# Performance work log

Measured on AMD Instinct MI355X. Metric: run time of the kernel, lower is better.

## Reference

```python
import jax, jax.numpy as jnp
import numpy as np

T, B, E, H = 1024, 2, 1024, 16
D = E // H


def setup_inputs() -> dict:
    key = jax.random.key(0)
    ks = jax.random.split(key, 5)
    s = 1.0 / np.sqrt(E)  # xavier_uniform bound ~ sqrt(6/(fan_in+fan_out)); scale suffices for a numeric baseline
    return {
        "query": jax.random.normal(ks[0], (T, B, E), jnp.float32),
        "key_": jax.random.normal(ks[1], (T, B, E), jnp.float32),
        "value": jax.random.normal(ks[2], (T, B, E), jnp.float32),
        "in_proj_weight": jax.random.uniform(ks[3], (3 * E, E), jnp.float32, -s, s),
        "in_proj_bias": jnp.zeros((3 * E,), jnp.float32),
        "out_proj_weight": jax.random.uniform(ks[4], (E, E), jnp.float32, -s, s),
        "out_proj_bias": jnp.zeros((E,), jnp.float32),
    }


def reference(query, key_, value, in_proj_weight, in_proj_bias, out_proj_weight, out_proj_bias):
    # Faithful to CumulativeLinearMultiheadAttentionKV.forward with
    # batch_first=False, is_causal=True, no padding mask, no kv cache.
    Tl, Bl, El = query.shape
    wq, wk, wv = jnp.split(in_proj_weight, 3, axis=0)
    bq, bk, bv = jnp.split(in_proj_bias, 3)
    q = query @ wq.T + bq          # (T, B, E)
    k = key_ @ wk.T + bk
    v = value @ wv.T + bv

    def to_bhtd(x):
        return x.reshape(Tl, Bl, H, D).transpose(1, 2, 0, 3)  # (B, H, T, D)

    q, k, v = to_bhtd(q), to_bhtd(k), to_bhtd(v)

    scale = 1.0 / np.sqrt(D)  # SDPA-style default scale (scale=None)
    # cumulative linear attention: prefix sums of k_s \otimes v_s
    kv = jnp.einsum('bhsk,bhsv->bhskv', k, v)        # (B, H, T, D, D)
    kv_store = jnp.cumsum(kv, axis=2)                # causal KV state per step
    out = jnp.einsum('bhtk,bhtkv->bhtv', q, kv_store) * scale  # (B, H, T, D)

    out = out.transpose(2, 0, 1, 3).reshape(Tl, Bl, El)  # back to (T, B, E)
    out = out @ out_proj_weight.T + out_proj_bias
    return out
```

## Files before the change

### kernel.cpp

```cpp
#include <hip/hip_runtime.h>


#define E_DIM 1024

typedef short bf16x8 __attribute__((ext_vector_type(8)));
typedef float f32x4  __attribute__((ext_vector_type(4)));

__device__ inline unsigned short f2bf(float f) {
    unsigned u = __builtin_bit_cast(unsigned, f);
    u = (u + 0x7FFFu + ((u >> 16) & 1u)) >> 16;
    return (unsigned short)u;
}

__device__ inline void gload_lds16(const void* g, void* l) {
    __builtin_amdgcn_global_load_lds(
        (const __attribute__((address_space(1))) unsigned int*)g,
        (__attribute__((address_space(3))) unsigned int*)l, 16, 0, 0);
}

__device__ inline int swzb(int row, int colbyte) {
    return colbyte ^ ((row & 7) << 4);
}

__global__ __launch_bounds__(256) void k_castw(
    const float* __restrict__ w_in, const float* __restrict__ w_out,
    unsigned short* __restrict__ dst)
{
    const int id8 = blockIdx.x * 256 + threadIdx.x;
    const int WI8 = 3 * E_DIM * E_DIM / 8;
    const float* src = (id8 < WI8) ? (w_in + (size_t)id8 * 8)
                                   : (w_out + (size_t)(id8 - WI8) * 8);
    float4 f0 = *reinterpret_cast<const float4*>(src);
    float4 f1 = *reinterpret_cast<const float4*>(src + 4);
    ushort4 o0, o1;
    o0.x = f2bf(f0.x); o0.y = f2bf(f0.y); o0.z = f2bf(f0.z); o0.w = f2bf(f0.w);
    o1.x = f2bf(f1.x); o1.y = f2bf(f1.y); o1.z = f2bf(f1.z); o1.w = f2bf(f1.w);
    *reinterpret_cast<ushort4*>(dst + (size_t)id8 * 8)     = o0;
    *reinterpret_cast<ushort4*>(dst + (size_t)id8 * 8 + 4) = o1;
}

__global__ __launch_bounds__(256) void k_gin(
    const float* __restrict__ q_in, const float* __restrict__ k_in,
    const float* __restrict__ v_in, const unsigned short* __restrict__ Wibf,
    const float* __restrict__ b_in,
    unsigned short* __restrict__ qslab, unsigned short* __restrict__ kslab,
    unsigned short* __restrict__ ktb,   unsigned short* __restrict__ vtb)
{
    const int i = blockIdx.x;
    const int tile = (i & 7) * 48 + (i >> 3);
    const int z = tile >> 7;
    const int rem = tile & 127;
    const int x = rem >> 5, y = rem & 31;

    const float* X = (z == 0) ? q_in : (z == 1 ? k_in : v_in);
    const unsigned short* W = Wibf + (size_t)z * 1048576;
    const float* bz = b_in + z * E_DIM;

    const int nBase = x * 256;
    const int mBase = y * 64;
    const int b = mBase >> 10, tBase = mBase & 1023;

    __shared__ short As[2][64 * 64];
    __shared__ short Bs[2][256 * 64];

    const int tid = threadIdx.x;
    const int lane = tid & 63, wave = tid >> 6;
    const int wr = wave >> 1, wc = wave & 1;
    const int l15 = lane & 15, l4 = lane >> 4;

    auto stage = [&](int bufI, int k0) {
        #pragma unroll
        for (int l = 0; l < 8; ++l) {
            int off = l * 4096 + tid * 16;
            int row = off >> 7, cb = off & 127;
            gload_lds16((const char*)W + ((size_t)(nBase + row) * E_DIM + k0) * 2
                            + swzb(row, cb),
                        (char*)&Bs[bufI][0] + off);
        }
        #pragma unroll
        for (int l = 0; l < 2; ++l) {
            int u = tid + 256 * l;
            int row = u >> 3, cslot = u & 7;
            const float* src = &X[(size_t)((tBase + row) * 2 + b) * E_DIM
                                  + k0 + cslot * 8];
            float4 f0 = *reinterpret_cast<const float4*>(src);
            float4 f1 = *reinterpret_cast<const float4*>(src + 4);
            bf16x8 p;
            p[0] = (short)f2bf(f0.x); p[1] = (short)f2bf(f0.y);
            p[2] = (short)f2bf(f0.z); p[3] = (short)f2bf(f0.w);
            p[4] = (short)f2bf(f1.x); p[5] = (short)f2bf(f1.y);
            p[6] = (short)f2bf(f1.z); p[7] = (short)f2bf(f1.w);
            *reinterpret_cast<bf16x8*>(
                &As[bufI][row * 64 + (swzb(row, cslot * 16) >> 1)]) = p;
        }
    };

    f32x4 acc[2][8] = {};

    stage(0, 0);
    __syncthreads();
    int cur = 0;
    for (int it = 0; it < 16; ++it) {
        if (it < 15) stage(cur ^ 1, (it + 1) * 64);
        #pragma unroll
        for (int kk = 0; kk < 64; kk += 32) {
            bf16x8 af[2], bfr[8];
            #pragma unroll
            for (int ii = 0; ii < 2; ++ii) {
                int row = wr * 32 + ii * 16 + l15;
                af[ii] = *reinterpret_cast<const bf16x8*>(
                    &As[cur][row * 64 + (swzb(row, (kk + l4 * 8) * 2) >> 1)]);
            }
            #pragma unroll
            for (int j = 0; j < 8; ++j) {
                int row = wc * 128 + j * 16 + l15;
                bfr[j] = *reinterpret_cast<const bf16x8*>(
                    &Bs[cur][row * 64 + (swzb(row, (kk + l4 * 8) * 2) >> 1)]);
            }
            #pragma unroll
            for (int ii = 0; ii < 2; ++ii)
                #pragma unroll
                for (int j = 0; j < 8; ++j)
                    acc[ii][j] = __builtin_amdgcn_mfma_f32_16x16x32_bf16(
                        af[ii], bfr[j], acc[ii][j], 0, 0, 0);
        }
        __syncthreads();
        cur ^= 1;
    }

    #pragma unroll
    for (int ii = 0; ii < 2; ++ii) {
        int t0 = tBase + wr * 32 + ii * 16 + l4 * 4;
        #pragma unroll
        for (int j = 0; j < 8; ++j) {
            int col = nBase + wc * 128 + j * 16 + l15;
            float bv = bz[col];
            unsigned short v4[4];
            #pragma unroll
            for (int q = 0; q < 4; ++q) v4[q] = f2bf(acc[ii][j][q] + bv);
            if (z == 0) {
                #pragma unroll
                for (int q = 0; q < 4; ++q)
                    qslab[(size_t)b * 1048576 + (size_t)(t0 + q) * E_DIM + col] = v4[q];
            } else if (z == 1) {
                #pragma unroll
                for (int q = 0; q < 4; ++q)
                    kslab[(size_t)b * 1048576 + (size_t)(t0 + q) * E_DIM + col] = v4[q];
                ushort4 w = {v4[0], v4[1], v4[2], v4[3]};
                *reinterpret_cast<ushort4*>(
                    &ktb[((size_t)b * 1024 + col) * 1024 + t0]) = w;
            } else {
                ushort4 w = {v4[0], v4[1], v4[2], v4[3]};
                *reinterpret_cast<ushort4*>(
                    &vtb[((size_t)b * 1024 + col) * 1024 + t0]) = w;
            }
        }
    }
}

__global__ __launch_bounds__(256) void k_attn(
    const unsigned short* __restrict__ qslab, const unsigned short* __restrict__ kslab,
    const unsigned short* __restrict__ ktb,  const unsigned short* __restrict__ vtb,
    unsigned short* __restrict__ attnbf)
{
    const int i = blockIdx.x;
    const int xcd = i & 7, u = i >> 3;
    const int bh = xcd * 4 + (u >> 4);
    const int qtr = u & 15;
    const int qt = ((u >> 5) & 1) ? (15 - qtr) : qtr;
    const int b = bh >> 4, h = bh & 15;
    const int colb = h * 64, t0q = qt * 64;

    __shared__ short Qs[64 * 64];
    __shared__ short KB[2][64 * 64];
    __shared__ short VB[2][64 * 64];
    __shared__ short Ss[64 * 72];
    __shared__ short PTs[64 * 72];

    const int tid = threadIdx.x;
    const int lane = tid & 63, wave = tid >> 6;
    const int wr = wave >> 1, wc = wave & 1;
    const int l15 = lane & 15, l4 = lane >> 4;

    auto stageP = [&](int bufI, int c) {
        int t0k = c * 64;
        #pragma unroll
        for (int l = 0; l < 2; ++l) {
            int off = l * 4096 + tid * 16;
            int row = off >> 7, cb = off & 127;
            int scb = swzb(row, cb);
            size_t trn = ((size_t)(b * 1024 + colb + row)) * 1024 + t0k;
            gload_lds16((const char*)ktb + trn * 2 + scb, (char*)&KB[bufI][0] + off);
            gload_lds16((const char*)vtb + trn * 2 + scb, (char*)&VB[bufI][0] + off);
        }
    };
    auto stageDiag = [&](int bufI) {
        #pragma unroll
        for (int l = 0; l < 2; ++l) {
            int off = l * 4096 + tid * 16;
            int row = off >> 7, cb = off & 127;
            int scb = swzb(row, cb);
            gload_lds16((const char*)kslab +
                            ((size_t)b * 1048576 + (size_t)(t0q + row) * E_DIM + colb) * 2 + scb,
                        (char*)&KB[bufI][0] + off);
            gload_lds16((const char*)vtb +
                            (((size_t)(b * 1024 + colb + row)) * 1024 + t0q) * 2 + scb,
                        (char*)&VB[bufI][0] + off);
        }
    };

    #pragma unroll
    for (int l = 0; l < 2; ++l) {
        int off = l * 4096 + tid * 16;
        int row = off >> 7, cb = off & 127;
        gload_lds16((const char*)qslab +
                        ((size_t)b * 1048576 + (size_t)(t0q + row) * E_DIM + colb) * 2
                        + swzb(row, cb),
                    (char*)Qs + off);
    }
    if (qt > 0) stageP(0, 0); else stageDiag(0);
    __syncthreads();

    f32x4 pacc[2][2] = {};
    int cur = 0;

    for (int c = 0; c < qt; ++c) {
        if (c + 1 < qt) stageP(cur ^ 1, c + 1); else stageDiag(cur ^ 1);
        #pragma unroll
        for (int kk = 0; kk < 64; kk += 32) {
            bf16x8 af[2], bfr[2];
            #pragma unroll
            for (int ii = 0; ii < 2; ++ii) {
                int row = wr * 32 + ii * 16 + l15;
                af[ii] = *reinterpret_cast<const bf16x8*>(
                    &KB[cur][row * 64 + (swzb(row, (kk + l4 * 8) * 2) >> 1)]);
            }
            #pragma unroll
            for (int j = 0; j < 2; ++j) {
                int row = wc * 32 + j * 16 + l15;
                bfr[j] = *reinterpret_cast<const bf16x8*>(
                    &VB[cur][row * 64 + (swzb(row, (kk + l4 * 8) * 2) >> 1)]);
            }
            #pragma unroll
            for (int ii = 0; ii < 2; ++ii)
                #pragma unroll
                for (int j = 0; j < 2; ++j)
                    pacc[ii][j] = __builtin_amdgcn_mfma_f32_16x16x32_bf16(
                        af[ii], bfr[j], pacc[ii][j], 0, 0, 0);
        }
        __syncthreads();
        cur ^= 1;
    }

    f32x4 sacc[2][2] = {};
    #pragma unroll
    for (int kk = 0; kk < 64; kk += 32) {
        bf16x8 af[2], bfr[2];
        #pragma unroll
        for (int ii = 0; ii < 2; ++ii) {
            int row = wr * 32 + ii * 16 + l15;
            af[ii] = *reinterpret_cast<const bf16x8*>(
                &Qs[row * 64 + (swzb(row, (kk + l4 * 8) * 2) >> 1)]);
        }
        #pragma unroll
        for (int j = 0; j < 2; ++j) {
            int row = wc * 32 + j * 16 + l15;
            bfr[j] = *reinterpret_cast<const bf16x8*>(
                &KB[cur][row * 64 + (swzb(row, (kk + l4 * 8) * 2) >> 1)]);
        }
        #pragma unroll
        for (int ii = 0; ii < 2; ++ii)
            #pragma unroll
            for (int j = 0; j < 2; ++j)
                sacc[ii][j] = __builtin_amdgcn_mfma_f32_16x16x32_bf16(
                    af[ii], bfr[j], sacc[ii][j], 0, 0, 0);
    }

    #pragma unroll
    for (int ii = 0; ii < 2; ++ii) {
        #pragma unroll
        for (int j = 0; j < 2; ++j) {
            int dv = wc * 32 + j * 16 + l15;
            int dkb = wr * 32 + ii * 16 + l4 * 4;
            ushort4 pw;
            pw.x = f2bf(pacc[ii][j][0]); pw.y = f2bf(pacc[ii][j][1]);
            pw.z = f2bf(pacc[ii][j][2]); pw.w = f2bf(pacc[ii][j][3]);
            *reinterpret_cast<ushort4*>(&PTs[dv * 72 + dkb]) = pw;
            int kr = dv;
            #pragma unroll
            for (int q = 0; q < 4; ++q) {
                int qr = dkb + q;
                Ss[qr * 72 + kr] = (kr <= qr) ? (short)f2bf(sacc[ii][j][q]) : (short)0;
            }
        }
    }
    __syncthreads();

    f32x4 oacc[2][2] = {};
    #pragma unroll
    for (int kk = 0; kk < 64; kk += 32) {
        bf16x8 af[2], bfr[2];
        #pragma unroll
        for (int ii = 0; ii < 2; ++ii)
            af[ii] = *reinterpret_cast<const bf16x8*>(
                        &Ss[(wr * 32 + ii * 16 + l15) * 72 + kk + l4 * 8]);
        #pragma unroll
        for (int j = 0; j < 2; ++j) {
            int row = wc * 32 + j * 16 + l15;
            bfr[j] = *reinterpret_cast<const bf16x8*>(
                &VB[cur][row * 64 + (swzb(row, (kk + l4 * 8) * 2) >> 1)]);
        }
        #pragma unroll
        for (int ii = 0; ii < 2; ++ii)
            #pragma unroll
            for (int j = 0; j < 2; ++j)
                oacc[ii][j] = __builtin_amdgcn_mfma_f32_16x16x32_bf16(
                    af[ii], bfr[j], oacc[ii][j], 0, 0, 0);
    }
    #pragma unroll
    for (int kk = 0; kk < 64; kk += 32) {
        bf16x8 af[2], bfr[2];
        #pragma unroll
        for (int ii = 0; ii < 2; ++ii) {
            int row = wr * 32 + ii * 16 + l15;
            af[ii] = *reinterpret_cast<const bf16x8*>(
                &Qs[row * 64 + (swzb(row, (kk + l4 * 8) * 2) >> 1)]);
        }
        #pragma unroll
        for (int j = 0; j < 2; ++j)
            bfr[j] = *reinterpret_cast<const bf16x8*>(
                        &PTs[(wc * 32 + j * 16 + l15) * 72 + kk + l4 * 8]);
        #pragma unroll
        for (int ii = 0; ii < 2; ++ii)
            #pragma unroll
            for (int j = 0; j < 2; ++j)
                oacc[ii][j] = __builtin_amdgcn_mfma_f32_16x16x32_bf16(
                    af[ii], bfr[j], oacc[ii][j], 0, 0, 0);
    }

    #pragma unroll
    for (int ii = 0; ii < 2; ++ii) {
        #pragma unroll
        for (int j = 0; j < 2; ++j) {
            int dv = wc * 32 + j * 16 + l15;
            #pragma unroll
            for (int q = 0; q < 4; ++q) {
                int qr = wr * 32 + ii * 16 + l4 * 4 + q;
                attnbf[(size_t)b * 1048576 + (size_t)(t0q + qr) * E_DIM + colb + dv] =
                    f2bf(oacc[ii][j][q] * 0.125f);
            }
        }
    }
}

__global__ __launch_bounds__(256) void k_gout(
    const unsigned short* __restrict__ attnbf, const unsigned short* __restrict__ Wobf,
    const float* __restrict__ bias, float* __restrict__ out)
{
    const int i = blockIdx.x;
    const int tile = (i & 7) * 64 + (i >> 3);
    const int x = tile & 15, y = tile >> 4;
    const int nBase = x * 64;
    const int mBase = y * 64;

    __shared__ short As[2][64 * 64];
    __shared__ short Bs[2][64 * 64];

    const int tid = threadIdx.x;
    const int lane = tid & 63, wave = tid >> 6;
    const int wr = wave >> 1, wc = wave & 1;
    const int l15 = lane & 15, l4 = lane >> 4;

    auto stage = [&](int bufI, int k0) {
        #pragma unroll
        for (int l = 0; l < 2; ++l) {
            int off = l * 4096 + tid * 16;
            int row = off >> 7, cb = off & 127;
            int scb = swzb(row, cb);
            gload_lds16((const char*)Wobf + ((size_t)(nBase + row) * E_DIM + k0) * 2 + scb,
                        (char*)&Bs[bufI][0] + off);
            int r = mBase + row, t = r >> 1, bb = r & 1;
            gload_lds16((const char*)attnbf +
                            ((size_t)bb * 1048576 + (size_t)t * E_DIM + k0) * 2 + scb,
                        (char*)&As[bufI][0] + off);
        }
    };

    f32x4 acc[2][2] = {};

    stage(0, 0);
    __syncthreads();
    int cur = 0;
    for (int it = 0; it < 16; ++it) {
        if (it < 15) stage(cur ^ 1, (it + 1) * 64);
        #pragma unroll
        for (int kk = 0; kk < 64; kk += 32) {
            bf16x8 af[2], bfr[2];
            #pragma unroll
            for (int ii = 0; ii < 2; ++ii) {
                int row = wr * 32 + ii * 16 + l15;
                af[ii] = *reinterpret_cast<const bf16x8*>(
                    &As[cur][row * 64 + (swzb(row, (kk + l4 * 8) * 2) >> 1)]);
            }
            #pragma unroll
            for (int j = 0; j < 2; ++j) {
                int row = wc * 32 + j * 16 + l15;
                bfr[j] = *reinterpret_cast<const bf16x8*>(
                    &Bs[cur][row * 64 + (swzb(row, (kk + l4 * 8) * 2) >> 1)]);
            }
            #pragma unroll
            for (int ii = 0; ii < 2; ++ii)
                #pragma unroll
                for (int j = 0; j < 2; ++j)
                    acc[ii][j] = __builtin_amdgcn_mfma_f32_16x16x32_bf16(
                        af[ii], bfr[j], acc[ii][j], 0, 0, 0);
        }
        __syncthreads();
        cur ^= 1;
    }

    #pragma unroll
    for (int ii = 0; ii < 2; ++ii) {
        int r0 = mBase + wr * 32 + ii * 16 + l4 * 4;
        #pragma unroll
        for (int j = 0; j < 2; ++j) {
            int col = nBase + wc * 32 + j * 16 + l15;
            float bv = bias[col];
            #pragma unroll
            for (int q = 0; q < 4; ++q)
                out[(size_t)(r0 + q) * E_DIM + col] = acc[ii][j][q] + bv;
        }
    }
}

extern "C" void kernel_launch(void* const* d_in, const int* in_sizes, int n_in,
                              void* d_out, int out_size, void* d_ws, size_t ws_size,
                              hipStream_t stream)
{
    const float* q_in  = (const float*)d_in[0];
    const float* k_in  = (const float*)d_in[1];
    const float* v_in  = (const float*)d_in[2];
    const float* w_in  = (const float*)d_in[3];
    const float* b_in  = (const float*)d_in[4];
    const float* w_out = (const float*)d_in[5];
    const float* b_out = (const float*)d_in[6];

    char* w = (char*)d_ws;
    unsigned short* Wibf   = (unsigned short*)w;
    unsigned short* Wobf   = (unsigned short*)(w + 6291456);
    unsigned short* qslab  = (unsigned short*)(w + 8388608);
    unsigned short* kslab  = (unsigned short*)(w + 12582912);
    unsigned short* vtb    = (unsigned short*)(w + 16777216);
    unsigned short* attnbf = (unsigned short*)(w + 20971520);
    unsigned short* ktb    = (unsigned short*)(w + 25165824);
    float* outp = (float*)d_out;

    k_castw<<<2048, 256, 0, stream>>>(w_in, w_out, Wibf);
    k_gin<<<384, 256, 0, stream>>>(q_in, k_in, v_in, Wibf, b_in,
                                   qslab, kslab, ktb, vtb);
    k_attn<<<512, 256, 0, stream>>>(qslab, kslab, ktb, vtb, attnbf);
    k_gout<<<512, 256, 0, stream>>>(attnbf, Wobf, b_out, outp);
}
```

Before: 147.9 us.

## Pre-cast activations to bf16 in cast kernel and stage them via direct LDS loads

The cast kernel now converts the q/k/v activations to bf16 along with both weight matrices, writing them into one contiguous workspace. The input-projection GEMM then loads A tiles with global_load_lds DMA instead of fp32 register loads followed by in-loop conversion, and its tile-to-XCD mapping is reordered. This removes the repeated fp32 loads and conversions in the GEMM inner loop, since each activation tile was otherwise converted once per N tile. The cost is an extra bf16 write and read pass over the activations in the cast kernel.

```diff
diff --git a/kernel.cpp b/kernel.cpp
--- a/kernel.cpp
+++ b/kernel.cpp
@@ -22,37 +22,43 @@
     return colbyte ^ ((row & 7) << 4);
 }
 
-__global__ __launch_bounds__(256) void k_castw(
-    const float* __restrict__ w_in, const float* __restrict__ w_out,
-    unsigned short* __restrict__ dst)
+__global__ __launch_bounds__(256) void k_cast(
+    const float* __restrict__ q_in, const float* __restrict__ k_in,
+    const float* __restrict__ v_in, const float* __restrict__ w_in,
+    const float* __restrict__ w_out, unsigned short* __restrict__ dst)
 {
-    const int id8 = blockIdx.x * 256 + threadIdx.x;
-    const int WI8 = 3 * E_DIM * E_DIM / 8;
-    const float* src = (id8 < WI8) ? (w_in + (size_t)id8 * 8)
-                                   : (w_out + (size_t)(id8 - WI8) * 8);
-    float4 f0 = *reinterpret_cast<const float4*>(src);
-    float4 f1 = *reinterpret_cast<const float4*>(src + 4);
-    ushort4 o0, o1;
-    o0.x = f2bf(f0.x); o0.y = f2bf(f0.y); o0.z = f2bf(f0.z); o0.w = f2bf(f0.w);
-    o1.x = f2bf(f1.x); o1.y = f2bf(f1.y); o1.z = f2bf(f1.z); o1.w = f2bf(f1.w);
-    *reinterpret_cast<ushort4*>(dst + (size_t)id8 * 8)     = o0;
-    *reinterpret_cast<ushort4*>(dst + (size_t)id8 * 8 + 4) = o1;
+    #pragma unroll
+    for (int l = 0; l < 4; ++l) {
+        int id8 = blockIdx.x * 256 + threadIdx.x + l * 327680;
+        const float* src;
+        if (id8 < 262144)        src = q_in  + (size_t)id8 * 8;
+        else if (id8 < 524288)   src = k_in  + (size_t)(id8 - 262144) * 8;
+        else if (id8 < 786432)   src = v_in  + (size_t)(id8 - 524288) * 8;
+        else if (id8 < 1179648)  src = w_in  + (size_t)(id8 - 786432) * 8;
+        else                     src = w_out + (size_t)(id8 - 1179648) * 8;
+        float4 f0 = *reinterpret_cast<const float4*>(src);
+        float4 f1 = *reinterpret_cast<const float4*>(src + 4);
+        ushort4 o0, o1;
+        o0.x = f2bf(f0.x); o0.y = f2bf(f0.y); o0.z = f2bf(f0.z); o0.w = f2bf(f0.w);
+        o1.x = f2bf(f1.x); o1.y = f2bf(f1.y); o1.z = f2bf(f1.z); o1.w = f2bf(f1.w);
+        *reinterpret_cast<ushort4*>(dst + (size_t)id8 * 8)     = o0;
+        *reinterpret_cast<ushort4*>(dst + (size_t)id8 * 8 + 4) = o1;
+    }
 }
 
 __global__ __launch_bounds__(256) void k_gin(
-    const float* __restrict__ q_in, const float* __restrict__ k_in,
-    const float* __restrict__ v_in, const unsigned short* __restrict__ Wibf,
+    const unsigned short* __restrict__ xbf, const unsigned short* __restrict__ Wibf,
     const float* __restrict__ b_in,
     unsigned short* __restrict__ qslab, unsigned short* __restrict__ kslab,
     unsigned short* __restrict__ ktb,   unsigned short* __restrict__ vtb)
 {
     const int i = blockIdx.x;
-    const int tile = (i & 7) * 48 + (i >> 3);
-    const int z = tile >> 7;
-    const int rem = tile & 127;
-    const int x = rem >> 5, y = rem & 31;
-
-    const float* X = (z == 0) ? q_in : (z == 1 ? k_in : v_in);
+    const int xcd = i & 7, j = i >> 3;
+    const int p = xcd * 12 + (j >> 2);
+    const int x = j & 3;
+    const int z = p >> 5, y = p & 31;
+
+    const unsigned short* X = xbf + (size_t)z * 2097152;
     const unsigned short* W = Wibf + (size_t)z * 1048576;
     const float* bz = b_in + z * E_DIM;
 
@@ -79,19 +85,12 @@
         }
         #pragma unroll
         for (int l = 0; l < 2; ++l) {
-            int u = tid + 256 * l;
-            int row = u >> 3, cslot = u & 7;
-            const float* src = &X[(size_t)((tBase + row) * 2 + b) * E_DIM
-                                  + k0 + cslot * 8];
-            float4 f0 = *reinterpret_cast<const float4*>(src);
-            float4 f1 = *reinterpret_cast<const float4*>(src + 4);
-            bf16x8 p;
-            p[0] = (short)f2bf(f0.x); p[1] = (short)f2bf(f0.y);
-            p[2] = (short)f2bf(f0.z); p[3] = (short)f2bf(f0.w);
-            p[4] = (short)f2bf(f1.x); p[5] = (short)f2bf(f1.y);
-            p[6] = (short)f2bf(f1.z); p[7] = (short)f2bf(f1.w);
-            *reinterpret_cast<bf16x8*>(
-                &As[bufI][row * 64 + (swzb(row, cslot * 16) >> 1)]) = p;
+            int off = l * 4096 + tid * 16;
+            int row = off >> 7, cb = off & 127;
+            gload_lds16((const char*)X +
+                            ((size_t)((tBase + row) * 2 + b) * E_DIM + k0) * 2
+                            + swzb(row, cb),
+                        (char*)&As[bufI][0] + off);
         }
     };
 
@@ -112,17 +111,17 @@
                     &As[cur][row * 64 + (swzb(row, (kk + l4 * 8) * 2) >> 1)]);
             }
             #pragma unroll
-            for (int j = 0; j < 8; ++j) {
-                int row = wc * 128 + j * 16 + l15;
-                bfr[j] = *reinterpret_cast<const bf16x8*>(
+            for (int jn = 0; jn < 8; ++jn) {
+                int row = wc * 128 + jn * 16 + l15;
+                bfr[jn] = *reinterpret_cast<const bf16x8*>(
                     &Bs[cur][row * 64 + (swzb(row, (kk + l4 * 8) * 2) >> 1)]);
             }
             #pragma unroll
             for (int ii = 0; ii < 2; ++ii)
                 #pragma unroll
-                for (int j = 0; j < 8; ++j)
-                    acc[ii][j] = __builtin_amdgcn_mfma_f32_16x16x32_bf16(
-                        af[ii], bfr[j], acc[ii][j], 0, 0, 0);
+                for (int jn = 0; jn < 8; ++jn)
+                    acc[ii][jn] = __builtin_amdgcn_mfma_f32_16x16x32_bf16(
+                        af[ii], bfr[jn], acc[ii][jn], 0, 0, 0);
         }
         __syncthreads();
         cur ^= 1;
@@ -132,12 +131,12 @@
     for (int ii = 0; ii < 2; ++ii) {
         int t0 = tBase + wr * 32 + ii * 16 + l4 * 4;
         #pragma unroll
-        for (int j = 0; j < 8; ++j) {
-            int col = nBase + wc * 128 + j * 16 + l15;
+        for (int jn = 0; jn < 8; ++jn) {
+            int col = nBase + wc * 128 + jn * 16 + l15;
             float bv = bz[col];
             unsigned short v4[4];
             #pragma unroll
-            for (int q = 0; q < 4; ++q) v4[q] = f2bf(acc[ii][j][q] + bv);
+            for (int q = 0; q < 4; ++q) v4[q] = f2bf(acc[ii][jn][q] + bv);
             if (z == 0) {
                 #pragma unroll
                 for (int q = 0; q < 4; ++q)
@@ -236,17 +235,17 @@
                     &KB[cur][row * 64 + (swzb(row, (kk + l4 * 8) * 2) >> 1)]);
             }
             #pragma unroll
-            for (int j = 0; j < 2; ++j) {
-                int row = wc * 32 + j * 16 + l15;
-                bfr[j] = *reinterpret_cast<const bf16x8*>(
+            for (int jn = 0; jn < 2; ++jn) {
+                int row = wc * 32 + jn * 16 + l15;
+                bfr[jn] = *reinterpret_cast<const bf16x8*>(
                     &VB[cur][row * 64 + (swzb(row, (kk + l4 * 8) * 2) >> 1)]);
             }
             #pragma unroll
             for (int ii = 0; ii < 2; ++ii)
                 #pragma unroll
-                for (int j = 0; j < 2; ++j)
-                    pacc[ii][j] = __builtin_amdgcn_mfma_f32_16x16x32_bf16(
-                        af[ii], bfr[j], pacc[ii][j], 0, 0, 0);
+                for (int jn = 0; jn < 2; ++jn)
+                    pacc[ii][jn] = __builtin_amdgcn_mfma_f32_16x16x32_bf16(
+                        af[ii], bfr[jn], pacc[ii][jn], 0, 0, 0);
         }
         __syncthreads();
         cur ^= 1;
@@ -263,34 +262,34 @@
                 &Qs[row * 64 + (swzb(row, (kk + l4 * 8) * 2) >> 1)]);
         }
         #pragma unroll
-        for (int j = 0; j < 2; ++j) {
-            int row = wc * 32 + j * 16 + l15;
-            bfr[j] = *reinterpret_cast<const bf16x8*>(
+        for (int jn = 0; jn < 2; ++jn) {
+            int row = wc * 32 + jn * 16 + l15;
+            bfr[jn] = *reinterpret_cast<const bf16x8*>(
                 &KB[cur][row * 64 + (swzb(row, (kk + l4 * 8) * 2) >> 1)]);
         }
         #pragma unroll
         for (int ii = 0; ii < 2; ++ii)
             #pragma unroll
-            for (int j = 0; j < 2; ++j)
-                sacc[ii][j] = __builtin_amdgcn_mfma_f32_16x16x32_bf16(
-                    af[ii], bfr[j], sacc[ii][j], 0, 0, 0);
+            for (int jn = 0; jn < 2; ++jn)
+                sacc[ii][jn] = __builtin_amdgcn_mfma_f32_16x16x32_bf16(
+                    af[ii], bfr[jn], sacc[ii][jn], 0, 0, 0);
     }
 
     #pragma unroll
     for (int ii = 0; ii < 2; ++ii) {
         #pragma unroll
-        for (int j = 0; j < 2; ++j) {
-            int dv = wc * 32 + j * 16 + l15;
+        for (int jn = 0; jn < 2; ++jn) {
+            int dv = wc * 32 + jn * 16 + l15;
             int dkb = wr * 32 + ii * 16 + l4 * 4;
             ushort4 pw;
-            pw.x = f2bf(pacc[ii][j][0]); pw.y = f2bf(pacc[ii][j][1]);
-            pw.z = f2bf(pacc[ii][j][2]); pw.w = f2bf(pacc[ii][j][3]);
+            pw.x = f2bf(pacc[ii][jn][0]); pw.y = f2bf(pacc[ii][jn][1]);
+            pw.z = f2bf(pacc[ii][jn][2]); pw.w = f2bf(pacc[ii][jn][3]);
             *reinterpret_cast<ushort4*>(&PTs[dv * 72 + dkb]) = pw;
             int kr = dv;
             #pragma unroll
             for (int q = 0; q < 4; ++q) {
                 int qr = dkb + q;
-                Ss[qr * 72 + kr] = (kr <= qr) ? (short)f2bf(sacc[ii][j][q]) : (short)0;
+                Ss[qr * 72 + kr] = (kr <= qr) ? (short)f2bf(sacc[ii][jn][q]) : (short)0;
             }
         }
     }
@@ -305,17 +304,17 @@
             af[ii] = *reinterpret_cast<const bf16x8*>(
                         &Ss[(wr * 32 + ii * 16 + l15) * 72 + kk + l4 * 8]);
         #pragma unroll
-        for (int j = 0; j < 2; ++j) {
-            int row = wc * 32 + j * 16 + l15;
-            bfr[j] = *reinterpret_cast<const bf16x8*>(
+        for (int jn = 0; jn < 2; ++jn) {
+            int row = wc * 32 + jn * 16 + l15;
+            bfr[jn] = *reinterpret_cast<const bf16x8*>(
                 &VB[cur][row * 64 + (swzb(row, (kk + l4 * 8) * 2) >> 1)]);
         }
         #pragma unroll
         for (int ii = 0; ii < 2; ++ii)
             #pragma unroll
-            for (int j = 0; j < 2; ++j)
-                oacc[ii][j] = __builtin_amdgcn_mfma_f32_16x16x32_bf16(
-                    af[ii], bfr[j], oacc[ii][j], 0, 0, 0);
+            for (int jn = 0; jn < 2; ++jn)
+                oacc[ii][jn] = __builtin_amdgcn_mfma_f32_16x16x32_bf16(
+                    af[ii], bfr[jn], oacc[ii][jn], 0, 0, 0);
     }
     #pragma unroll
     for (int kk = 0; kk < 64; kk += 32) {
@@ -327,27 +326,27 @@
                 &Qs[row * 64 + (swzb(row, (kk + l4 * 8) * 2) >> 1)]);
         }
         #pragma unroll
-        for (int j = 0; j < 2; ++j)
-            bfr[j] = *reinterpret_cast<const bf16x8*>(
-                        &PTs[(wc * 32 + j * 16 + l15) * 72 + kk + l4 * 8]);
+        for (int jn = 0; jn < 2; ++jn)
+            bfr[jn] = *reinterpret_cast<const bf16x8*>(
+                        &PTs[(wc * 32 + jn * 16 + l15) * 72 + kk + l4 * 8]);
         #pragma unroll
         for (int ii = 0; ii < 2; ++ii)
             #pragma unroll
-            for (int j = 0; j < 2; ++j)
-                oacc[ii][j] = __builtin_amdgcn_mfma_f32_16x16x32_bf16(
-                    af[ii], bfr[j], oacc[ii][j], 0, 0, 0);
+            for (int jn = 0; jn < 2; ++jn)
+                oacc[ii][jn] = __builtin_amdgcn_mfma_f32_16x16x32_bf16(
+                    af[ii], bfr[jn], oacc[ii][jn], 0, 0, 0);
     }
 
     #pragma unroll
     for (int ii = 0; ii < 2; ++ii) {
         #pragma unroll
-        for (int j = 0; j < 2; ++j) {
-            int dv = wc * 32 + j * 16 + l15;
+        for (int jn = 0; jn < 2; ++jn) {
+            int dv = wc * 32 + jn * 16 + l15;
             #pragma unroll
             for (int q = 0; q < 4; ++q) {
                 int qr = wr * 32 + ii * 16 + l4 * 4 + q;
                 attnbf[(size_t)b * 1048576 + (size_t)(t0q + qr) * E_DIM + colb + dv] =
-                    f2bf(oacc[ii][j][q] * 0.125f);
+                    f2bf(oacc[ii][jn][q] * 0.125f);
             }
         }
     }
@@ -403,17 +402,17 @@
                     &As[cur][row * 64 + (swzb(row, (kk + l4 * 8) * 2) >> 1)]);
             }
             #pragma unroll
-            for (int j = 0; j < 2; ++j) {
-                int row = wc * 32 + j * 16 + l15;
-                bfr[j] = *reinterpret_cast<const bf16x8*>(
+            for (int jn = 0; jn < 2; ++jn) {
+                int row = wc * 32 + jn * 16 + l15;
+                bfr[jn] = *reinterpret_cast<const bf16x8*>(
                     &Bs[cur][row * 64 + (swzb(row, (kk + l4 * 8) * 2) >> 1)]);
             }
             #pragma unroll
             for (int ii = 0; ii < 2; ++ii)
                 #pragma unroll
-                for (int j = 0; j < 2; ++j)
-                    acc[ii][j] = __builtin_amdgcn_mfma_f32_16x16x32_bf16(
-                        af[ii], bfr[j], acc[ii][j], 0, 0, 0);
+                for (int jn = 0; jn < 2; ++jn)
+                    acc[ii][jn] = __builtin_amdgcn_mfma_f32_16x16x32_bf16(
+                        af[ii], bfr[jn], acc[ii][jn], 0, 0, 0);
         }
         __syncthreads();
         cur ^= 1;
@@ -423,12 +422,12 @@
     for (int ii = 0; ii < 2; ++ii) {
         int r0 = mBase + wr * 32 + ii * 16 + l4 * 4;
         #pragma unroll
-        for (int j = 0; j < 2; ++j) {
-            int col = nBase + wc * 32 + j * 16 + l15;
+        for (int jn = 0; jn < 2; ++jn) {
+            int col = nBase + wc * 32 + jn * 16 + l15;
             float bv = bias[col];
             #pragma unroll
             for (int q = 0; q < 4; ++q)
-                out[(size_t)(r0 + q) * E_DIM + col] = acc[ii][j][q] + bv;
+                out[(size_t)(r0 + q) * E_DIM + col] = acc[ii][jn][q] + bv;
         }
     }
 }
@@ -446,18 +445,18 @@
     const float* b_out = (const float*)d_in[6];
 
     char* w = (char*)d_ws;
-    unsigned short* Wibf   = (unsigned short*)w;
-    unsigned short* Wobf   = (unsigned short*)(w + 6291456);
-    unsigned short* qslab  = (unsigned short*)(w + 8388608);
-    unsigned short* kslab  = (unsigned short*)(w + 12582912);
-    unsigned short* vtb    = (unsigned short*)(w + 16777216);
-    unsigned short* attnbf = (unsigned short*)(w + 20971520);
-    unsigned short* ktb    = (unsigned short*)(w + 25165824);
+    unsigned short* xbf    = (unsigned short*)w;
+    unsigned short* Wibf   = (unsigned short*)(w + 12582912);
+    unsigned short* Wobf   = (unsigned short*)(w + 18874368);
+    unsigned short* qslab  = (unsigned short*)(w + 20971520);
+    unsigned short* kslab  = (unsigned short*)(w + 25165824);
+    unsigned short* ktb    = (unsigned short*)(w + 29360128);
+    unsigned short* vtb    = (unsigned short*)(w + 33554432);
+    unsigned short* attnbf = (unsigned short*)(w + 37748736);
     float* outp = (float*)d_out;
 
-    k_castw<<<2048, 256, 0, stream>>>(w_in, w_out, Wibf);
-    k_gin<<<384, 256, 0, stream>>>(q_in, k_in, v_in, Wibf, b_in,
-                                   qslab, kslab, ktb, vtb);
+    k_cast<<<1280, 256, 0, stream>>>(q_in, k_in, v_in, w_in, w_out, xbf);
+    k_gin<<<384, 256, 0, stream>>>(xbf, Wibf, b_in, qslab, kslab, ktb, vtb);
     k_attn<<<512, 256, 0, stream>>>(qslab, kslab, ktb, vtb, attnbf);
     k_gout<<<512, 256, 0, stream>>>(attnbf, Wobf, b_out, outp);
 }
```

Measured after the change: 145.9 us. Within noise of the previous version (-1.3%).
